# Optimization experiments

Hardware: AMD Instinct MI355X
Metric: run time of the kernel (lower is better)

The kernel has to match this reference:

```python
import jax, jax.numpy as jnp
import numpy as np

N_NODES = 100000
N_EDGES = 3200000
IN_F, HID, NC = 384, 64, 2


def setup_inputs() -> dict:
    key = jax.random.key(0)
    ks = jax.random.split(key, 8)
    X = jax.random.normal(ks[0], (N_NODES, IN_F), dtype=jnp.float32)
    edge_index = jax.random.randint(ks[1], (2, N_EDGES), 0, N_NODES, dtype=jnp.int64)
    edge_weight = jax.random.uniform(ks[2], (N_EDGES,), dtype=jnp.float32)
    W1 = jax.random.normal(ks[3], (IN_F, HID), dtype=jnp.float32) / np.sqrt(IN_F)
    b1 = jnp.zeros((HID,), dtype=jnp.float32)
    W2 = jax.random.normal(ks[4], (HID, HID), dtype=jnp.float32) / np.sqrt(HID)
    b2 = jnp.zeros((HID,), dtype=jnp.float32)
    Wm1 = jax.random.normal(ks[5], (HID, HID), dtype=jnp.float32) / np.sqrt(HID)
    bm1 = jnp.zeros((HID,), dtype=jnp.float32)
    Wm2 = jax.random.normal(ks[6], (HID, NC), dtype=jnp.float32) / np.sqrt(HID)
    bm2 = jnp.zeros((NC,), dtype=jnp.float32)
    return {"X": X, "edge_index": edge_index, "edge_weight": edge_weight,
            "W1": W1, "b1": b1, "W2": W2, "b2": b2,
            "Wm1": Wm1, "bm1": bm1, "Wm2": Wm2, "bm2": bm2}


def _gcn_norm(edge_index, edge_weight, n):
    # add self-loops with weight 1 (PyG gcn_norm, add_self_loops=True)
    loop = jnp.arange(n, dtype=edge_index.dtype)
    row = jnp.concatenate([edge_index[0], loop])
    col = jnp.concatenate([edge_index[1], loop])
    w = jnp.concatenate([edge_weight, jnp.ones((n,), edge_weight.dtype)])
    deg = jax.ops.segment_sum(w, col, num_segments=n)
    dis = jnp.where(deg > 0, jax.lax.rsqrt(jnp.where(deg > 0, deg, 1.0)), 0.0)
    norm = dis[row] * w * dis[col]  # [E+N]
    return row, col, norm


def _gcn_conv(x, row, col, norm, W, b, n):
    h = x @ W                                   # [N, out]
    msg = norm[:, None] * h[row]                # gather + scale  [E+N, out]
    return jax.ops.segment_sum(msg, col, num_segments=n) + b


def reference(X, edge_index, edge_weight, W1, b1, W2, b2, Wm1, bm1, Wm2, bm2):
    n = X.shape[0]
    row, col, norm = _gcn_norm(edge_index, edge_weight, n)
    # PyG BasicGNN: act (leaky_relu) after all but last conv; dropout off in eval
    h = _gcn_conv(X, row, col, norm, W1, b1, n)
    h = jax.nn.leaky_relu(h, negative_slope=0.01)
    h = _gcn_conv(h, row, col, norm, W2, b2, n)
    # MLP: Linear -> Dropout(eval: identity) -> ELU -> Linear
    h = jax.nn.elu(h @ Wm1 + bm1)
    logits = h @ Wm2 + bm2
    return jax.nn.softmax(logits, axis=-1)
```

## Files before the change

kernel.cpp:

```cpp
#include <hip/hip_runtime.h>
#include <math.h>

#define NN 100000
#define NE 3200000
#define INF 384
#define HID 64
#define CAP 48
#define OVF_CAP 65536
#define NBIN 391
#define NREP 8
#define NCTR (NBIN * NREP)
#define BCAP 1536
#define EPB 8192
#define NBLK ((NE + EPB - 1) / EPB)

typedef unsigned long long ulong64;
typedef unsigned int uint32;
typedef unsigned short ushort16;
typedef __attribute__((ext_vector_type(8))) short bf16x8;
typedef __attribute__((ext_vector_type(4))) float f32x4;

__device__ inline float bf16_to_f(uint32 us) { return __uint_as_float(us << 16); }
__device__ inline ushort16 f_to_bf16(float f) {
    uint32 u = __float_as_uint(f);
    u += 0x7FFF + ((u >> 16) & 1);
    return (ushort16)(u >> 16);
}
__device__ inline void split_bf16(float x, ushort16& h, ushort16& l) {
    h = f_to_bf16(x);
    float hf = bf16_to_f((uint32)h);
    l = f_to_bf16(x - hf);
}


__global__ __launch_bounds__(256) void setup_kernel(const float* __restrict__ W1,
                                                    const float* __restrict__ W2,
                                                    const float* __restrict__ Wm1,
                                                    ushort16* __restrict__ wp1h,
                                                    ushort16* __restrict__ wp1l,
                                                    ushort16* __restrict__ wp2h,
                                                    ushort16* __restrict__ wp2l,
                                                    ushort16* __restrict__ wpm1h,
                                                    ushort16* __restrict__ wpm1l,
                                                    int* __restrict__ ovf_cnt,
                                                    int* __restrict__ bincur) {
    int i = blockIdx.x * blockDim.x + threadIdx.x;
    int np = gridDim.x * blockDim.x;
    if (i == 0) *ovf_cnt = 0;
    for (int idx = i; idx < NCTR; idx += np) bincur[idx] = idx * BCAP;
    for (int idx = i; idx < INF * HID; idx += np) {
        int k = idx >> 6, j = idx & 63;
        ushort16 h, l;
        split_bf16(W1[idx], h, l);
        size_t dst = ((size_t)(((k >> 5) * 4 + (j >> 4)) * 64 +
                               ((j & 15) | (((k >> 3) & 3) << 4))) << 3) + (k & 7);
        wp1h[dst] = h;
        wp1l[dst] = l;
    }
    for (int idx = i; idx < HID * HID; idx += np) {
        int k = idx >> 6, j = idx & 63;
        size_t dst = ((size_t)(((k >> 5) * 4 + (j >> 4)) * 64 +
                               ((j & 15) | (((k >> 3) & 3) << 4))) << 3) + (k & 7);
        ushort16 h, l;
        split_bf16(W2[idx], h, l);
        wp2h[dst] = h;
        wp2l[dst] = l;
        split_bf16(Wm1[idx], h, l);
        wpm1h[dst] = h;
        wpm1l[dst] = l;
    }
}


__global__ __launch_bounds__(1024) void binscatter_kernel(const int* __restrict__ row,
                                                          const int* __restrict__ col,
                                                          const float* __restrict__ ew,
                                                          int* __restrict__ bincur,
                                                          ulong64* __restrict__ ebin) {
    __shared__ int lhist[NBIN];
    __shared__ int lbase[NBIN];
    int tid = threadIdx.x;
    int rep = blockIdx.x & (NREP - 1);
    int base = blockIdx.x * EPB;
    if (tid < NBIN) lhist[tid] = 0;
    __syncthreads();
    int brk[8], rr[8];
    uint32 wb[8];
#pragma unroll
    for (int i = 0; i < 8; i++) {
        int e = base + i * 1024 + tid;
        brk[i] = -1;
        if (e < NE) {
            int r = row[e];
            int c = col[e];
            wb[i] = __float_as_uint(ew[e]);
            int b = c >> 8;
            int rk = atomicAdd(&lhist[b], 1);
            brk[i] = (b << 16) | rk;
            rr[i] = r | ((c & 255) << 17);
        }
    }
    __syncthreads();
    if (tid < NBIN && lhist[tid] > 0)
        lbase[tid] = atomicAdd(&bincur[tid * NREP + rep], lhist[tid]);
    __syncthreads();
#pragma unroll
    for (int i = 0; i < 8; i++) {
        if (brk[i] >= 0) {
            int b = brk[i] >> 16;
            int pos = lbase[b] + (brk[i] & 0xFFFF);
            int lim = (b * NREP + rep + 1) * BCAP;
            if (pos < lim)
                ebin[pos] = ((ulong64)wb[i] << 32) | (uint32)rr[i];
        }
    }
}


__global__ __launch_bounds__(256) void bucket_kernel(const int* __restrict__ bincur,
                                                     const ulong64* __restrict__ ebin,
                                                     ulong64* __restrict__ sedge,
                                                     int* __restrict__ cnt,
                                                     float* __restrict__ dis,
                                                     int* __restrict__ ovf_cnt,
                                                     int4* __restrict__ ovf) {
    __shared__ int cur[256];
    __shared__ float sdeg[256];
    int bin = blockIdx.x;
    int node0 = bin << 8;
    cur[threadIdx.x] = 0;
    sdeg[threadIdx.x] = 0.f;
    __syncthreads();
    for (int rep = 0; rep < NREP; rep++) {
        int ctr = bin * NREP + rep;
        int start = ctr * BCAP;
        int end = min(bincur[ctr], start + BCAP);
        for (int i = start + threadIdx.x; i < end; i += 256) {
            ulong64 pk = ebin[i];
            int r = (int)(pk & 0x1FFFF);
            int lc = (int)((pk >> 17) & 255);
            uint32 wb = (uint32)(pk >> 32);
            atomicAdd(&sdeg[lc], __uint_as_float(wb));
            int rank = atomicAdd(&cur[lc], 1);
            int node = node0 + lc;
            if (rank < CAP) {
                sedge[(size_t)node * CAP + rank] = ((ulong64)wb << 32) | (uint32)r;
            } else {
                int o = atomicAdd(ovf_cnt, 1);
                if (o < OVF_CAP) ovf[o] = make_int4(r, node, (int)wb, 0);
            }
        }
    }
    __syncthreads();
    int node = node0 + threadIdx.x;
    if (node < NN) {
        int cc = min(cur[threadIdx.x], CAP);
        cnt[node] = cc;
        int cpad = min((cc + 7) & ~7, CAP);
        for (int s = cc; s < cpad; s++) sedge[(size_t)node * CAP + s] = 0;
        dis[node] = rsqrtf(sdeg[threadIdx.x] + 1.0f);
    }
}


template <int K, bool LEAKY>
__global__ __launch_bounds__(256, 6) void mfma_gemm_kernel(const float* __restrict__ A,
                                                           const ushort16* __restrict__ Wph,
                                                           const ushort16* __restrict__ Wpl,
                                                           const float* __restrict__ dis,
                                                           ushort16* __restrict__ out) {
    __shared__ ushort16 Xh[64][72];
    __shared__ ushort16 Xl[64][72];
    const int tid = threadIdx.x;
    const int nb = blockIdx.x * 64;
    const int w = tid >> 6;
    const int l = tid & 63;
    const int lrow = l & 15;
    const int lkb = (l >> 4) * 8;
    const bf16x8* __restrict__ Bh = (const bf16x8*)Wph;
    const bf16x8* __restrict__ Bl = (const bf16x8*)Wpl;

    f32x4 acc[4];
#pragma unroll
    for (int n = 0; n < 4; n++) acc[n] = (f32x4){0.f, 0.f, 0.f, 0.f};

    constexpr int NT = K / 64;
    float4 vreg[4];

#pragma unroll
    for (int t = 0; t < 4; t++) {
        int f = t * 256 + tid;
        int rr = f >> 4;
        int c4 = f & 15;
        int gr = nb + rr;
        vreg[t] = make_float4(0.f, 0.f, 0.f, 0.f);
        if (gr < NN) vreg[t] = *(const float4*)&A[(size_t)gr * K + c4 * 4];
    }

#pragma unroll
    for (int kt = 0; kt < NT; kt++) {
#pragma unroll
        for (int t = 0; t < 4; t++) {
            int f = t * 256 + tid;
            int rr = f >> 4;
            int c4 = f & 15;
            float4 v = vreg[t];
            if (LEAKY) {
                v.x = v.x > 0.f ? v.x : 0.01f * v.x;
                v.y = v.y > 0.f ? v.y : 0.01f * v.y;
                v.z = v.z > 0.f ? v.z : 0.01f * v.z;
                v.w = v.w > 0.f ? v.w : 0.01f * v.w;
            }
            ushort4 oh, ol;
            split_bf16(v.x, oh.x, ol.x);
            split_bf16(v.y, oh.y, ol.y);
            split_bf16(v.z, oh.z, ol.z);
            split_bf16(v.w, oh.w, ol.w);
            *(ushort4*)&Xh[rr][c4 * 4] = oh;
            *(ushort4*)&Xl[rr][c4 * 4] = ol;
        }
        __syncthreads();
        if (kt + 1 < NT) {
#pragma unroll
            for (int t = 0; t < 4; t++) {
                int f = t * 256 + tid;
                int rr = f >> 4;
                int c4 = f & 15;
                int gr = nb + rr;
                vreg[t] = make_float4(0.f, 0.f, 0.f, 0.f);
                if (gr < NN)
                    vreg[t] = *(const float4*)&A[(size_t)gr * K + (kt + 1) * 64 + c4 * 4];
            }
        }
#pragma unroll
        for (int ks = 0; ks < 2; ks++) {
            int ktl = ks * 32 + lkb;
            int kslot = kt * 2 + ks;
            bf16x8 ah = *(const bf16x8*)&Xh[w * 16 + lrow][ktl];
            bf16x8 al = *(const bf16x8*)&Xl[w * 16 + lrow][ktl];
#pragma unroll
            for (int n = 0; n < 4; n++) {
                bf16x8 bh = Bh[(size_t)(kslot * 4 + n) * 64 + l];
                bf16x8 bl = Bl[(size_t)(kslot * 4 + n) * 64 + l];
                acc[n] = __builtin_amdgcn_mfma_f32_16x16x32_bf16(ah, bh, acc[n], 0, 0, 0);
                acc[n] = __builtin_amdgcn_mfma_f32_16x16x32_bf16(al, bh, acc[n], 0, 0, 0);
                acc[n] = __builtin_amdgcn_mfma_f32_16x16x32_bf16(ah, bl, acc[n], 0, 0, 0);
            }
        }
        __syncthreads();
    }
    int rbase = nb + w * 16 + (l >> 4) * 4;
#pragma unroll
    for (int r = 0; r < 4; r++) {
        int node = rbase + r;
        if (node < NN) {
            float ds = dis[node];
#pragma unroll
            for (int n = 0; n < 4; n++)
                out[(size_t)node * HID + n * 16 + lrow] = f_to_bf16(acc[n][r] * ds);
        }
    }
}


__global__ __launch_bounds__(256) void aggregate_kernel(const int* __restrict__ cnt,
                                                        const ulong64* __restrict__ sedge,
                                                        const float* __restrict__ dis,
                                                        const ushort16* __restrict__ hs,
                                                        const float* __restrict__ bias,
                                                        float* __restrict__ out) {
    int lane = threadIdx.x & 63;
    int wslot = __builtin_amdgcn_readfirstlane(threadIdx.x >> 6);
    int n = blockIdx.x * 4 + wslot;
    if (n >= NN) return;
    int c = cnt[n];
    int cpad = (c + 7) & ~7;
    float dn = dis[n];
    const ulong64* __restrict__ el = sedge + (size_t)n * CAP;

    float acc = bf16_to_f((uint32)hs[(size_t)n * HID + lane]);
    if (cpad > 0) {
        ulong64 p[8];
#pragma unroll
        for (int i = 0; i < 8; i++) p[i] = el[i];
        int j = 0;
        for (;;) {
            int jn = j + 8;
            bool more = jn < cpad;
            ulong64 q[8];
            if (more) {
#pragma unroll
                for (int i = 0; i < 8; i++) q[i] = el[jn + i];
            }
            float v[8], wv[8];
#pragma unroll
            for (int i = 0; i < 8; i++) {
                uint32 r = (uint32)p[i];
                wv[i] = __uint_as_float((uint32)(p[i] >> 32));
                v[i] = bf16_to_f((uint32)hs[(size_t)r * HID + lane]);
            }
#pragma unroll
            for (int i = 0; i < 8; i++) acc = fmaf(wv[i], v[i], acc);
            if (!more) break;
            j = jn;
#pragma unroll
            for (int i = 0; i < 8; i++) p[i] = q[i];
        }
    }
    out[(size_t)n * HID + lane] = fmaf(dn, acc, bias[lane]);
}


__global__ __launch_bounds__(256) void ovf_kernel(const int* __restrict__ ovf_cnt,
                                                  const int4* __restrict__ ovf,
                                                  const float* __restrict__ dis,
                                                  const ushort16* __restrict__ hs,
                                                  float* __restrict__ out) {
    int lane = threadIdx.x & 63;
    int wid = blockIdx.x * 4 + (threadIdx.x >> 6);
    int nw = gridDim.x * 4;
    int c = min(*ovf_cnt, OVF_CAP);
    for (int i = wid; i < c; i += nw) {
        int4 t = ovf[i];
        float w = __int_as_float(t.z);
        float nrm = w * dis[t.y];
        atomicAdd(&out[(size_t)t.y * HID + lane],
                  nrm * bf16_to_f((uint32)hs[(size_t)t.x * HID + lane]));
    }
}


__global__ __launch_bounds__(256) void mlp_mfma_kernel(const float* __restrict__ agg,
                                                       const ushort16* __restrict__ Wph,
                                                       const ushort16* __restrict__ Wpl,
                                                       const float* __restrict__ bm1,
                                                       const float* __restrict__ Wm2,
                                                       const float* __restrict__ bm2,
                                                       float* __restrict__ out) {
    __shared__ ushort16 Xh[64][72];
    __shared__ ushort16 Xl[64][72];
    const int tid = threadIdx.x;
    const int nb = blockIdx.x * 64;
    const int w = tid >> 6;
    const int l = tid & 63;
    const int lrow = l & 15;
    const int lkb = (l >> 4) * 8;
    const bf16x8* __restrict__ Bh = (const bf16x8*)Wph;
    const bf16x8* __restrict__ Bl = (const bf16x8*)Wpl;

#pragma unroll
    for (int t = 0; t < 4; t++) {
        int f = t * 256 + tid;
        int rr = f >> 4;
        int c4 = f & 15;
        int gr = nb + rr;
        float4 v = make_float4(0.f, 0.f, 0.f, 0.f);
        if (gr < NN) v = *(const float4*)&agg[(size_t)gr * HID + c4 * 4];
        ushort4 oh, ol;
        split_bf16(v.x, oh.x, ol.x);
        split_bf16(v.y, oh.y, ol.y);
        split_bf16(v.z, oh.z, ol.z);
        split_bf16(v.w, oh.w, ol.w);
        *(ushort4*)&Xh[rr][c4 * 4] = oh;
        *(ushort4*)&Xl[rr][c4 * 4] = ol;
    }
    __syncthreads();

    f32x4 acc[4];
#pragma unroll
    for (int n = 0; n < 4; n++) acc[n] = (f32x4){0.f, 0.f, 0.f, 0.f};

#pragma unroll
    for (int ks = 0; ks < 2; ks++) {
        bf16x8 ah = *(const bf16x8*)&Xh[w * 16 + lrow][ks * 32 + lkb];
        bf16x8 al = *(const bf16x8*)&Xl[w * 16 + lrow][ks * 32 + lkb];
#pragma unroll
        for (int n = 0; n < 4; n++) {
            bf16x8 bh = Bh[(size_t)(ks * 4 + n) * 64 + l];
            bf16x8 bl = Bl[(size_t)(ks * 4 + n) * 64 + l];
            acc[n] = __builtin_amdgcn_mfma_f32_16x16x32_bf16(ah, bh, acc[n], 0, 0, 0);
            acc[n] = __builtin_amdgcn_mfma_f32_16x16x32_bf16(al, bh, acc[n], 0, 0, 0);
            acc[n] = __builtin_amdgcn_mfma_f32_16x16x32_bf16(ah, bl, acc[n], 0, 0, 0);
        }
    }

    float b1c[4], w2a[4], w2b[4];
#pragma unroll
    for (int n = 0; n < 4; n++) {
        int colw = n * 16 + lrow;
        b1c[n] = bm1[colw];
        w2a[n] = Wm2[colw * 2];
        w2b[n] = Wm2[colw * 2 + 1];
    }
    float b20 = bm2[0], b21 = bm2[1];

#pragma unroll
    for (int r = 0; r < 4; r++) {
        float s0 = 0.f, s1 = 0.f;
#pragma unroll
        for (int n = 0; n < 4; n++) {
            float u = acc[n][r] + b1c[n];
            u = u > 0.f ? u : (expf(u) - 1.f);
            s0 = fmaf(u, w2a[n], s0);
            s1 = fmaf(u, w2b[n], s1);
        }
#pragma unroll
        for (int off = 1; off < 16; off <<= 1) {
            s0 += __shfl_xor(s0, off);
            s1 += __shfl_xor(s1, off);
        }
        int node = nb + w * 16 + (l >> 4) * 4 + r;
        if (lrow == 0 && node < NN) {
            float l0 = s0 + b20, l1 = s1 + b21;
            float m = fmaxf(l0, l1);
            float e0 = expf(l0 - m), e1 = expf(l1 - m);
            float inv = 1.f / (e0 + e1);
            *(float2*)&out[(size_t)node * 2] = make_float2(e0 * inv, e1 * inv);
        }
    }
}


extern "C" void kernel_launch(void* const* d_in, const int* in_sizes, int n_in,
                              void* d_out, int out_size, void* d_ws, size_t ws_size,
                              hipStream_t stream) {
    const float* X   = (const float*)d_in[0];
    const int*   ei  = (const int*)d_in[1];
    const float* ew  = (const float*)d_in[2];
    const float* W1  = (const float*)d_in[3];
    const float* b1  = (const float*)d_in[4];
    const float* W2  = (const float*)d_in[5];
    const float* b2  = (const float*)d_in[6];
    const float* Wm1 = (const float*)d_in[7];
    const float* bm1 = (const float*)d_in[8];
    const float* Wm2 = (const float*)d_in[9];
    const float* bm2 = (const float*)d_in[10];
    const int* row = ei;
    const int* col = ei + NE;
    float* out = (float*)d_out;

    const size_t MB = 1024 * 1024;
    const size_t KB = 1024;
    char* ws = (char*)d_ws;
    float*    dis     = (float*)   (ws + 0 * MB);
    int*      cnt     = (int*)     (ws + 1 * MB);
    ushort16* wp1h    = (ushort16*)(ws + 2 * MB);
    ushort16* wp1l    = (ushort16*)(ws + 2 * MB + 64 * KB);
    ushort16* wp2h    = (ushort16*)(ws + 2 * MB + 128 * KB);
    ushort16* wp2l    = (ushort16*)(ws + 2 * MB + 144 * KB);
    ushort16* wpm1h   = (ushort16*)(ws + 2 * MB + 160 * KB);
    ushort16* wpm1l   = (ushort16*)(ws + 2 * MB + 176 * KB);
    int*      ovf_cnt = (int*)     (ws + 3 * MB);
    int*      bincur  = (int*)     (ws + 3 * MB + 16 * KB);
    int4*     ovf     = (int4*)    (ws + 4 * MB);
    ulong64*  ebin    = (ulong64*) (ws + 5 * MB);
    float*    h2      = (float*)   (ws + 5 * MB);
    ulong64*  sedge   = (ulong64*) (ws + 44 * MB);
    ushort16* h1      = (ushort16*)(ws + 83 * MB);

    setup_kernel<<<64, 256, 0, stream>>>(W1, W2, Wm1, wp1h, wp1l, wp2h, wp2l,
                                         wpm1h, wpm1l, ovf_cnt, bincur);
    binscatter_kernel<<<NBLK, 1024, 0, stream>>>(row, col, ew, bincur, ebin);
    bucket_kernel<<<NBIN, 256, 0, stream>>>(bincur, ebin, sedge, cnt, dis, ovf_cnt, ovf);

    mfma_gemm_kernel<INF, false><<<(NN + 63) / 64, 256, 0, stream>>>(X, wp1h, wp1l, dis, h1);
    aggregate_kernel<<<(NN + 3) / 4, 256, 0, stream>>>(cnt, sedge, dis, h1, b1, h2);
    ovf_kernel<<<256, 256, 0, stream>>>(ovf_cnt, ovf, dis, h1, h2);

    mfma_gemm_kernel<HID, true><<<(NN + 63) / 64, 256, 0, stream>>>(h2, wp2h, wp2l, dis, h1);
    aggregate_kernel<<<(NN + 3) / 4, 256, 0, stream>>>(cnt, sedge, dis, h1, b2, h2);
    ovf_kernel<<<256, 256, 0, stream>>>(ovf_cnt, ovf, dis, h1, h2);

    mlp_mfma_kernel<<<(NN + 63) / 64, 256, 0, stream>>>(h2, wpm1h, wpm1l, bm1, Wm2, bm2, out);
}
```

Measured before the change: 495.9 us.

## Load MFMA A-fragments directly from global memory, dropping LDS staging

The GEMM and MLP kernels now have each lane load its own 8-element A fragment straight from global memory, convert it to hi/lo bf16 in registers and feed the MFMA. This removes the shared-memory tiles and the __syncthreads barriers. A one-step register prefetch of the next K-slice is kept. Launch bounds change to 4 waves/SIMD. The trade-off is less coalesced global access: each lane reads 32 contiguous bytes per row rather than whole rows, which may add memory transactions.

```diff
diff --git a/kernel.cpp b/kernel.cpp
--- a/kernel.cpp
+++ b/kernel.cpp
@@ -164,90 +164,58 @@
 
 
 template <int K, bool LEAKY>
-__global__ __launch_bounds__(256, 6) void mfma_gemm_kernel(const float* __restrict__ A,
+__global__ __launch_bounds__(256, 4) void mfma_gemm_kernel(const float* __restrict__ A,
                                                            const ushort16* __restrict__ Wph,
                                                            const ushort16* __restrict__ Wpl,
                                                            const float* __restrict__ dis,
                                                            ushort16* __restrict__ out) {
-    __shared__ ushort16 Xh[64][72];
-    __shared__ ushort16 Xl[64][72];
     const int tid = threadIdx.x;
-    const int nb = blockIdx.x * 64;
     const int w = tid >> 6;
     const int l = tid & 63;
     const int lrow = l & 15;
-    const int lkb = (l >> 4) * 8;
+    const int nb = blockIdx.x * 64;
+    const int row = nb + w * 16 + lrow;
+    const int kq = (l >> 4) * 8;
     const bf16x8* __restrict__ Bh = (const bf16x8*)Wph;
     const bf16x8* __restrict__ Bl = (const bf16x8*)Wpl;
+    const float* __restrict__ arow = A + (size_t)min(row, NN - 1) * K + kq;
 
     f32x4 acc[4];
 #pragma unroll
     for (int n = 0; n < 4; n++) acc[n] = (f32x4){0.f, 0.f, 0.f, 0.f};
 
-    constexpr int NT = K / 64;
-    float4 vreg[4];
-
-#pragma unroll
-    for (int t = 0; t < 4; t++) {
-        int f = t * 256 + tid;
-        int rr = f >> 4;
-        int c4 = f & 15;
-        int gr = nb + rr;
-        vreg[t] = make_float4(0.f, 0.f, 0.f, 0.f);
-        if (gr < NN) vreg[t] = *(const float4*)&A[(size_t)gr * K + c4 * 4];
-    }
-
-#pragma unroll
-    for (int kt = 0; kt < NT; kt++) {
-#pragma unroll
-        for (int t = 0; t < 4; t++) {
-            int f = t * 256 + tid;
-            int rr = f >> 4;
-            int c4 = f & 15;
-            float4 v = vreg[t];
-            if (LEAKY) {
-                v.x = v.x > 0.f ? v.x : 0.01f * v.x;
-                v.y = v.y > 0.f ? v.y : 0.01f * v.y;
-                v.z = v.z > 0.f ? v.z : 0.01f * v.z;
-                v.w = v.w > 0.f ? v.w : 0.01f * v.w;
-            }
-            ushort4 oh, ol;
-            split_bf16(v.x, oh.x, ol.x);
-            split_bf16(v.y, oh.y, ol.y);
-            split_bf16(v.z, oh.z, ol.z);
-            split_bf16(v.w, oh.w, ol.w);
-            *(ushort4*)&Xh[rr][c4 * 4] = oh;
-            *(ushort4*)&Xl[rr][c4 * 4] = ol;
-        }
-        __syncthreads();
-        if (kt + 1 < NT) {
-#pragma unroll
-            for (int t = 0; t < 4; t++) {
-                int f = t * 256 + tid;
-                int rr = f >> 4;
-                int c4 = f & 15;
-                int gr = nb + rr;
-                vreg[t] = make_float4(0.f, 0.f, 0.f, 0.f);
-                if (gr < NN)
-                    vreg[t] = *(const float4*)&A[(size_t)gr * K + (kt + 1) * 64 + c4 * 4];
-            }
-        }
-#pragma unroll
-        for (int ks = 0; ks < 2; ks++) {
-            int ktl = ks * 32 + lkb;
-            int kslot = kt * 2 + ks;
-            bf16x8 ah = *(const bf16x8*)&Xh[w * 16 + lrow][ktl];
-            bf16x8 al = *(const bf16x8*)&Xl[w * 16 + lrow][ktl];
-#pragma unroll
-            for (int n = 0; n < 4; n++) {
-                bf16x8 bh = Bh[(size_t)(kslot * 4 + n) * 64 + l];
-                bf16x8 bl = Bl[(size_t)(kslot * 4 + n) * 64 + l];
-                acc[n] = __builtin_amdgcn_mfma_f32_16x16x32_bf16(ah, bh, acc[n], 0, 0, 0);
-                acc[n] = __builtin_amdgcn_mfma_f32_16x16x32_bf16(al, bh, acc[n], 0, 0, 0);
-                acc[n] = __builtin_amdgcn_mfma_f32_16x16x32_bf16(ah, bl, acc[n], 0, 0, 0);
-            }
-        }
-        __syncthreads();
+    constexpr int NS = K / 32;
+    float4 a0 = *(const float4*)(arow);
+    float4 a1 = *(const float4*)(arow + 4);
+#pragma unroll
+    for (int ks = 0; ks < NS; ks++) {
+        float4 p0 = make_float4(0.f, 0.f, 0.f, 0.f);
+        float4 p1 = p0;
+        if (ks + 1 < NS) {
+            p0 = *(const float4*)(arow + (ks + 1) * 32);
+            p1 = *(const float4*)(arow + (ks + 1) * 32 + 4);
+        }
+        float av[8] = {a0.x, a0.y, a0.z, a0.w, a1.x, a1.y, a1.z, a1.w};
+        bf16x8 ah, al;
+#pragma unroll
+        for (int i = 0; i < 8; i++) {
+            float x = av[i];
+            if (LEAKY) x = x > 0.f ? x : 0.01f * x;
+            ushort16 hh, ll;
+            split_bf16(x, hh, ll);
+            ah[i] = (short)hh;
+            al[i] = (short)ll;
+        }
+#pragma unroll
+        for (int n = 0; n < 4; n++) {
+            bf16x8 bh = Bh[(size_t)(ks * 4 + n) * 64 + l];
+            bf16x8 bl = Bl[(size_t)(ks * 4 + n) * 64 + l];
+            acc[n] = __builtin_amdgcn_mfma_f32_16x16x32_bf16(ah, bh, acc[n], 0, 0, 0);
+            acc[n] = __builtin_amdgcn_mfma_f32_16x16x32_bf16(al, bh, acc[n], 0, 0, 0);
+            acc[n] = __builtin_amdgcn_mfma_f32_16x16x32_bf16(ah, bl, acc[n], 0, 0, 0);
+        }
+        a0 = p0;
+        a1 = p1;
     }
     int rbase = nb + w * 16 + (l >> 4) * 4;
 #pragma unroll
@@ -330,41 +298,23 @@
 }
 
 
-__global__ __launch_bounds__(256) void mlp_mfma_kernel(const float* __restrict__ agg,
-                                                       const ushort16* __restrict__ Wph,
-                                                       const ushort16* __restrict__ Wpl,
-                                                       const float* __restrict__ bm1,
-                                                       const float* __restrict__ Wm2,
-                                                       const float* __restrict__ bm2,
-                                                       float* __restrict__ out) {
-    __shared__ ushort16 Xh[64][72];
-    __shared__ ushort16 Xl[64][72];
+__global__ __launch_bounds__(256, 4) void mlp_mfma_kernel(const float* __restrict__ agg,
+                                                          const ushort16* __restrict__ Wph,
+                                                          const ushort16* __restrict__ Wpl,
+                                                          const float* __restrict__ bm1,
+                                                          const float* __restrict__ Wm2,
+                                                          const float* __restrict__ bm2,
+                                                          float* __restrict__ out) {
     const int tid = threadIdx.x;
-    const int nb = blockIdx.x * 64;
     const int w = tid >> 6;
     const int l = tid & 63;
     const int lrow = l & 15;
-    const int lkb = (l >> 4) * 8;
+    const int nb = blockIdx.x * 64;
+    const int row = nb + w * 16 + lrow;
+    const int kq = (l >> 4) * 8;
     const bf16x8* __restrict__ Bh = (const bf16x8*)Wph;
     const bf16x8* __restrict__ Bl = (const bf16x8*)Wpl;
-
-#pragma unroll
-    for (int t = 0; t < 4; t++) {
-        int f = t * 256 + tid;
-        int rr = f >> 4;
-        int c4 = f & 15;
-        int gr = nb + rr;
-        float4 v = make_float4(0.f, 0.f, 0.f, 0.f);
-        if (gr < NN) v = *(const float4*)&agg[(size_t)gr * HID + c4 * 4];
-        ushort4 oh, ol;
-        split_bf16(v.x, oh.x, ol.x);
-        split_bf16(v.y, oh.y, ol.y);
-        split_bf16(v.z, oh.z, ol.z);
-        split_bf16(v.w, oh.w, ol.w);
-        *(ushort4*)&Xh[rr][c4 * 4] = oh;
-        *(ushort4*)&Xl[rr][c4 * 4] = ol;
-    }
-    __syncthreads();
+    const float* __restrict__ arow = agg + (size_t)min(row, NN - 1) * HID + kq;
 
     f32x4 acc[4];
 #pragma unroll
@@ -372,8 +322,17 @@
 
 #pragma unroll
     for (int ks = 0; ks < 2; ks++) {
-        bf16x8 ah = *(const bf16x8*)&Xh[w * 16 + lrow][ks * 32 + lkb];
-        bf16x8 al = *(const bf16x8*)&Xl[w * 16 + lrow][ks * 32 + lkb];
+        float4 a0 = *(const float4*)(arow + ks * 32);
+        float4 a1 = *(const float4*)(arow + ks * 32 + 4);
+        float av[8] = {a0.x, a0.y, a0.z, a0.w, a1.x, a1.y, a1.z, a1.w};
+        bf16x8 ah, al;
+#pragma unroll
+        for (int i = 0; i < 8; i++) {
+            ushort16 hh, ll;
+            split_bf16(av[i], hh, ll);
+            ah[i] = (short)hh;
+            al[i] = (short)ll;
+        }
 #pragma unroll
         for (int n = 0; n < 4; n++) {
             bf16x8 bh = Bh[(size_t)(ks * 4 + n) * 64 + l];
```

After: 500.4 us. About the same (+0.9%).
